# Kernel optimization log

Measured on AMD Instinct MI355X. Metric: run time of the kernel, lower is better.

The kernel has to match this reference:

```python
import jax, jax.numpy as jnp
import numpy as np

GN_GROUPS = 32
GN_EPS = 1e-5


def conv1x1(x, w, b):
    # x: [B,C,H,W], w: [O,C], b: [O]
    return jnp.einsum('bchw,oc->bohw', x, w) + b[None, :, None, None]


def maxpool2(x):
    B, C, H, W = x.shape
    return x.reshape(B, C, H // 2, 2, W // 2, 2).max(axis=(3, 5))


def group_norm(x, w, b, groups=GN_GROUPS, eps=GN_EPS):
    B, C, H, W = x.shape
    xg = x.reshape(B, groups, -1)
    m = xg.mean(axis=-1, keepdims=True)
    v = xg.var(axis=-1, keepdims=True)
    xn = ((xg - m) * jax.lax.rsqrt(v + eps)).reshape(B, C, H, W)
    return xn * w[None, :, None, None] + b[None, :, None, None]


def setup_inputs() -> dict:
    key = jax.random.key(0)
    ks = jax.random.split(key, 8)
    B, C, Ci, H, W = 4, 128, 64, 96, 96
    s_in = 1.0 / np.sqrt(C)
    s_ic = 1.0 / np.sqrt(Ci)
    return {
        'x': jax.random.normal(ks[0], (B, C, H, W), jnp.float32),
        'w_theta': jax.random.normal(ks[1], (Ci, C), jnp.float32) * s_in,
        'b_theta': jnp.zeros((Ci,), jnp.float32),
        'w_phi': jax.random.normal(ks[2], (Ci, C), jnp.float32) * s_in,
        'b_phi': jnp.zeros((Ci,), jnp.float32),
        'w_g': jax.random.normal(ks[3], (Ci, C), jnp.float32) * s_in,
        'b_g': jnp.zeros((Ci,), jnp.float32),
        'w_W': jax.random.normal(ks[4], (C, Ci), jnp.float32) * s_ic,
        'b_W': jnp.zeros((C,), jnp.float32),
        'gn_w': jnp.ones((C,), jnp.float32),
        'gn_b': jnp.zeros((C,), jnp.float32),
    }


def reference(x, w_theta, b_theta, w_phi, b_phi, w_g, b_g, w_W, b_W, gn_w, gn_b):
    B, C, H, W = x.shape
    Ci = w_theta.shape[0]
    # projections (1x1 convs); phi and g are 2x2 max-pooled (sub_sample=True)
    theta = conv1x1(x, w_theta, b_theta).reshape(B, Ci, H * W)          # [B,Ci,N]
    phi = maxpool2(conv1x1(x, w_phi, b_phi)).reshape(B, Ci, -1)         # [B,Ci,N']
    g = maxpool2(conv1x1(x, w_g, b_g)).reshape(B, Ci, -1)               # [B,Ci,N']
    # unscaled single-head attention
    f = jnp.einsum('bcn,bcm->bnm', theta, phi)                          # [B,N,N']
    f = jax.nn.softmax(f, axis=-1)
    y = jnp.einsum('bnm,bcm->bcn', f, g).reshape(B, Ci, H, W)           # [B,Ci,H,W]
    w_y = group_norm(conv1x1(y, w_W, b_W), gn_w, gn_b)
    return w_y + x
```

## Files before the change

kernel.cpp:

```cpp
#include <hip/hip_runtime.h>
#include <math.h>

#define B_ 4
#define C_ 128
#define CI_ 64
#define H_ 96
#define W_ 96
#define HW_ (H_*W_)
#define NP_ 2304
#define GROUPS_ 32
#define EPS_ 1e-5f
#define KVT_ 32
#define NT_ (NP_/KVT_)
#define NBLK_ 288

typedef _Float16 f16x8 __attribute__((ext_vector_type(8)));
typedef _Float16 f16x2 __attribute__((ext_vector_type(2)));
typedef __attribute__((ext_vector_type(4))) float f32x4;

__device__ inline f32x4 mfma16h(f16x8 a, f16x8 b, f32x4 c) {
    return __builtin_amdgcn_mfma_f32_16x16x32_f16(a, b, c, 0, 0, 0);
}
__device__ inline float h2f(unsigned short s) {
    return (float)__builtin_bit_cast(_Float16, s);
}
__device__ inline unsigned pk_f16(float a, float b) {
    return __builtin_bit_cast(unsigned, __builtin_amdgcn_cvt_pkrtz(a, b));
}
__device__ inline f16x8 pk8(float v0, float v1, float v2, float v3,
                            float v4, float v5, float v6, float v7) {
    uint4 u = { pk_f16(v0, v1), pk_f16(v2, v3), pk_f16(v4, v5), pk_f16(v6, v7) };
    return __builtin_bit_cast(f16x8, u);
}
__device__ inline unsigned short hmax4(unsigned short a, unsigned short b,
                                       unsigned short c, unsigned short d) {
    unsigned short m = (h2f(a) >= h2f(b)) ? a : b;
    unsigned short n = (h2f(c) >= h2f(d)) ? c : d;
    return (h2f(m) >= h2f(n)) ? m : n;
}
__device__ inline void gload_lds16(const void* g, void* l) {
    __builtin_amdgcn_global_load_lds(
        (const __attribute__((address_space(1))) void*)reinterpret_cast<uintptr_t>(g),
        (__attribute__((address_space(3))) void*)(unsigned)reinterpret_cast<uintptr_t>(l),
        16, 0, 0);
}

__global__ __launch_bounds__(256) void wprep_kernel(
    const float* __restrict__ w_theta, const float* __restrict__ w_phi,
    const float* __restrict__ w_g,     const float* __restrict__ w_W,
    unsigned short* __restrict__ Whall)
{
    const int idx = blockIdx.x * 256 + threadIdx.x;
    float v;
    if      (idx <  8192) v = w_theta[idx];
    else if (idx < 16384) v = w_phi[idx - 8192];
    else if (idx < 24576) v = w_g[idx - 16384];
    else                  v = w_W[idx - 24576];
    Whall[idx] = __builtin_bit_cast(unsigned short, (_Float16)v);
}

__global__ __launch_bounds__(128) void proj_kernel(
    const float* __restrict__ x, const unsigned short* __restrict__ Whall,
    const float* __restrict__ b_theta, const float* __restrict__ b_phi,
    const float* __restrict__ b_g,
    unsigned short* __restrict__ Qo, unsigned short* __restrict__ Ko,
    unsigned short* __restrict__ Vt)
{
    __shared__ __align__(16) unsigned short pb[2][16 * 72];

    const int t    = threadIdx.x;
    const int wv   = t >> 6;
    const int lane = t & 63;
    const int lr   = lane & 15;
    const int lg   = lane >> 4;
    const int b    = blockIdx.y;
    const int h0   = (blockIdx.x / 6) * 2;
    const int w0   = (blockIdx.x % 6) * 16;
    const int nb   = (h0 + wv) * W_ + w0;
    const int m0   = (h0 >> 1) * 48 + (w0 >> 1);

    const float* xb = x + (size_t)b * C_ * HW_ + nb + lr;
    f16x8 xa[4];
    #pragma unroll
    for (int u = 0; u < 4; ++u) {
        const float* p = xb + (size_t)(u * 32 + lg * 8) * HW_;
        xa[u] = pk8(p[0], p[(size_t)HW_], p[2 * (size_t)HW_], p[3 * (size_t)HW_],
                    p[4 * (size_t)HW_], p[5 * (size_t)HW_], p[6 * (size_t)HW_],
                    p[7 * (size_t)HW_]);
    }

    #pragma unroll
    for (int mat = 0; mat < 3; ++mat) {
        const unsigned short* Whp = Whall + mat * 8192;
        const float* bsel = (mat == 0) ? b_theta : (mat == 1) ? b_phi : b_g;

        f32x4 D[4];
        #pragma unroll
        for (int ct = 0; ct < 4; ++ct) D[ct] = (f32x4){0.f, 0.f, 0.f, 0.f};
        #pragma unroll
        for (int u = 0; u < 4; ++u)
            #pragma unroll
            for (int ct = 0; ct < 4; ++ct) {
                f16x8 wb = *(const f16x8*)&Whp[(ct * 16 + lr) * 128 + u * 32 + lg * 8];
                D[ct] = mfma16h(xa[u], wb, D[ct]);
            }

        #pragma unroll
        for (int ct = 0; ct < 4; ++ct) {
            const float bi = bsel[ct * 16 + lr];
            #pragma unroll
            for (int r2 = 0; r2 < 4; ++r2)
                pb[wv][(4 * lg + r2) * 72 + ct * 16 + lr] =
                    __builtin_bit_cast(unsigned short, (_Float16)(D[ct][r2] + bi));
        }

        if (mat == 0) {
            const int px = lane >> 2, ch = lane & 3;
            f16x8 y0 = *(const f16x8*)&pb[wv][px * 72 + ch * 16];
            f16x8 y1 = *(const f16x8*)&pb[wv][px * 72 + ch * 16 + 8];
            unsigned short* op = Qo + ((size_t)b * HW_ + nb + px) * CI_ + ch * 16;
            *(f16x8*)op       = y0;
            *(f16x8*)(op + 8) = y1;
        } else if (mat == 1) {
            __syncthreads();
            const int w = t >> 4, ci0 = (t & 15) * 4;
            unsigned short r[4];
            #pragma unroll
            for (int j = 0; j < 4; ++j) {
                const int ci = ci0 + j;
                r[j] = hmax4(pb[0][(2 * w) * 72 + ci], pb[0][(2 * w + 1) * 72 + ci],
                             pb[1][(2 * w) * 72 + ci], pb[1][(2 * w + 1) * 72 + ci]);
            }
            *(ushort4*)&Ko[((size_t)b * NP_ + m0 + w) * CI_ + ci0] =
                (ushort4){r[0], r[1], r[2], r[3]};
            __syncthreads();
        } else {
            __syncthreads();
            const int ci = t >> 1, pr = t & 1;
            #pragma unroll
            for (int j = 0; j < 4; ++j) {
                const int w = pr * 4 + j;
                unsigned short v = hmax4(
                    pb[0][(2 * w) * 72 + ci], pb[0][(2 * w + 1) * 72 + ci],
                    pb[1][(2 * w) * 72 + ci], pb[1][(2 * w + 1) * 72 + ci]);
                const int m  = m0 + w;
                const int ms = (m & ~31)
                             | (8 * ((m >> 2) & 3) + 4 * ((m >> 4) & 1) + (m & 3));
                Vt[((size_t)b * CI_ + ci) * NP_ + ms] = v;
            }
        }
    }
}

__global__ __launch_bounds__(128) void attn_kernel(
    const unsigned short* __restrict__ Qg, const unsigned short* __restrict__ Kg,
    const unsigned short* __restrict__ Vt, const unsigned short* __restrict__ wWh,
    const float* __restrict__ bW, unsigned short* __restrict__ Zh,
    float* __restrict__ gpart)
{
    __shared__ unsigned char Klds[2][4096];
    __shared__ unsigned char Vlds[2][4096];

    const int t    = threadIdx.x;
    const int wv   = t >> 6;
    const int lane = t & 63;
    const int lr   = lane & 15;
    const int lg   = lane >> 4;
    const int b    = blockIdx.y;
    const int q0   = blockIdx.x * 32 + wv * 16;

    const int krow = lane >> 3;
    const int kchk = (lane & 7) ^ krow;
    const int vrow = lane >> 2;
    const int vchk = (lane & 3) ^ (vrow & 3);

    const unsigned short* Kb = Kg + (size_t)b * NP_ * CI_;
    const unsigned short* Vb = Vt + (size_t)b * CI_ * NP_;

    f16x8 qf[2];
    #pragma unroll
    for (int u = 0; u < 2; ++u)
        qf[u] = *(const f16x8*)(Qg + ((size_t)b * HW_ + q0 + lr) * CI_ + u * 32 + lg * 8);

    f32x4 o_acc[4];
    #pragma unroll
    for (int dt = 0; dt < 4; ++dt) o_acc[dt] = (f32x4){0.f, 0.f, 0.f, 0.f};
    float mrun = -1e30f, lrun = 0.f;

#define STAGE(BUF, TT)                                                          \
    {                                                                           \
        const int kv0_ = (TT) * KVT_;                                           \
        if (wv == 0) {                                                          \
            _Pragma("unroll")                                                   \
            for (int i = 0; i < 4; ++i)                                         \
                gload_lds16(Kb + (size_t)(kv0_ + 8 * i + krow) * CI_ + kchk * 8,\
                            &Klds[BUF][i * 1024]);                              \
        } else {                                                                \
            _Pragma("unroll")                                                   \
            for (int i = 0; i < 4; ++i)                                         \
                gload_lds16(Vb + (size_t)(16 * i + vrow) * NP_ + kv0_ + vchk * 8,\
                            &Vlds[BUF][i * 1024]);                              \
        }                                                                       \
    }

#define COMPUTE(BUF)                                                            \
    {                                                                           \
        f16x8 kf[2][2];                                                         \
        _Pragma("unroll")                                                       \
        for (int u = 0; u < 2; ++u)                                             \
            _Pragma("unroll")                                                   \
            for (int k4 = 0; k4 < 2; ++k4)                                      \
                kf[u][k4] = *(const f16x8*)&Klds[BUF][(k4 * 16 + lr) * 128      \
                                + (((4 * u + lg) ^ (lr & 7)) << 4)];            \
        f32x4 s[2];                                                             \
        s[0] = (f32x4){0.f, 0.f, 0.f, 0.f};                                     \
        s[1] = (f32x4){0.f, 0.f, 0.f, 0.f};                                     \
        __builtin_amdgcn_s_setprio(1);                                          \
        _Pragma("unroll")                                                       \
        for (int u = 0; u < 2; ++u) {                                           \
            s[0] = mfma16h(kf[u][0], qf[u], s[0]);                              \
            s[1] = mfma16h(kf[u][1], qf[u], s[1]);                              \
        }                                                                       \
        __builtin_amdgcn_s_setprio(0);                                          \
        float tmax = fmaxf(fmaxf(fmaxf(s[0][0], s[0][1]),                       \
                                 fmaxf(s[0][2], s[0][3])),                      \
                           fmaxf(fmaxf(s[1][0], s[1][1]),                       \
                                 fmaxf(s[1][2], s[1][3])));                     \
        if (!__all(tmax <= mrun + 8.0f)) {                                      \
            tmax = fmaxf(tmax, __shfl_xor(tmax, 16));                           \
            tmax = fmaxf(tmax, __shfl_xor(tmax, 32));                           \
            const float mnew = fmaxf(mrun, tmax);                               \
            const float sc = __expf(mrun - mnew);                               \
            lrun *= sc;                                                         \
            _Pragma("unroll")                                                   \
            for (int r2 = 0; r2 < 4; ++r2) {                                    \
                const float scb = __shfl(sc, 4 * lg + r2);                      \
                _Pragma("unroll")                                               \
                for (int dt = 0; dt < 4; ++dt) o_acc[dt][r2] *= scb;            \
            }                                                                   \
            mrun = mnew;                                                        \
        }                                                                       \
        const float e00 = __expf(s[0][0] - mrun);                               \
        const float e01 = __expf(s[0][1] - mrun);                               \
        const float e02 = __expf(s[0][2] - mrun);                               \
        const float e03 = __expf(s[0][3] - mrun);                               \
        const float e10 = __expf(s[1][0] - mrun);                               \
        const float e11 = __expf(s[1][1] - mrun);                               \
        const float e12 = __expf(s[1][2] - mrun);                               \
        const float e13 = __expf(s[1][3] - mrun);                               \
        lrun += ((e00 + e01) + (e02 + e03)) + ((e10 + e11) + (e12 + e13));      \
        f16x8 pf = pk8(e00, e01, e02, e03, e10, e11, e12, e13);                 \
        __builtin_amdgcn_s_setprio(1);                                          \
        _Pragma("unroll")                                                       \
        for (int dt = 0; dt < 4; ++dt) {                                        \
            const int vrow_ = dt * 16 + lr;                                     \
            f16x8 vf = *(const f16x8*)&Vlds[BUF][vrow_ * 64                     \
                            + (((lg ^ (lr & 3))) << 4)];                        \
            o_acc[dt] = mfma16h(pf, vf, o_acc[dt]);                             \
        }                                                                       \
        __builtin_amdgcn_s_setprio(0);                                          \
    }

    STAGE(0, 0);
    STAGE(1, 1);

    for (int it = 0; it < NT_ / 2; ++it) {
        const int t0 = 2 * it;
        asm volatile("s_waitcnt vmcnt(4)" ::: "memory");
        __builtin_amdgcn_s_barrier();
        COMPUTE(0);
        __builtin_amdgcn_s_barrier();
        if (t0 + 2 < NT_) STAGE(0, t0 + 2);
        if (it == NT_ / 2 - 1) {
            asm volatile("s_waitcnt vmcnt(0)" ::: "memory");
        } else {
            asm volatile("s_waitcnt vmcnt(4)" ::: "memory");
        }
        __builtin_amdgcn_s_barrier();
        COMPUTE(1);
        __builtin_amdgcn_s_barrier();
        if (t0 + 3 < NT_) STAGE(1, t0 + 3);
    }

    float lt = lrun;
    lt += __shfl_xor(lt, 16);
    lt += __shfl_xor(lt, 32);
    unsigned short* yb = (unsigned short*)&Klds[wv][0];
    #pragma unroll
    for (int r2 = 0; r2 < 4; ++r2) {
        const float inv = 1.0f / __shfl(lt, 4 * lg + r2);
        #pragma unroll
        for (int dt = 0; dt < 4; ++dt)
            yb[(4 * lg + r2) * 72 + dt * 16 + lr] =
                __builtin_bit_cast(unsigned short, (_Float16)(o_acc[dt][r2] * inv));
    }

    float* wpart = (float*)&Vlds[0][0];
    f16x8 ya[2];
    #pragma unroll
    for (int u = 0; u < 2; ++u)
        ya[u] = *(const f16x8*)&yb[lr * 72 + u * 32 + lg * 8];

    unsigned short* Zb = Zh + (size_t)b * C_ * HW_ + q0 + lr;
    #pragma unroll
    for (int ot = 0; ot < 8; ++ot) {
        f32x4 D = (f32x4){0.f, 0.f, 0.f, 0.f};
        #pragma unroll
        for (int u = 0; u < 2; ++u) {
            f16x8 wa = *(const f16x8*)&wWh[(ot * 16 + lr) * CI_ + u * 32 + lg * 8];
            D = mfma16h(wa, ya[u], D);
        }
        float zs = 0.f, zq = 0.f;
        #pragma unroll
        for (int r2 = 0; r2 < 4; ++r2) {
            const int o = ot * 16 + 4 * lg + r2;
            const float z = D[r2] + bW[o];
            Zb[(size_t)o * HW_] = __builtin_bit_cast(unsigned short, (_Float16)z);
            zs += z;
            zq += z * z;
        }
        zs += __shfl_xor(zs, 1);  zq += __shfl_xor(zq, 1);
        zs += __shfl_xor(zs, 2);  zq += __shfl_xor(zq, 2);
        zs += __shfl_xor(zs, 4);  zq += __shfl_xor(zq, 4);
        zs += __shfl_xor(zs, 8);  zq += __shfl_xor(zq, 8);
        if (lr == 0) {
            wpart[(wv * 32 + ot * 4 + lg) * 2 + 0] = zs;
            wpart[(wv * 32 + ot * 4 + lg) * 2 + 1] = zq;
        }
    }
    __syncthreads();
    if (t < 64) {
        const int g = t >> 1, w = t & 1;
        const float v = wpart[(g) * 2 + w] + wpart[(32 + g) * 2 + w];
        gpart[(((size_t)b * NBLK_ + blockIdx.x) * 32 + g) * 2 + w] = v;
    }
#undef STAGE
#undef COMPUTE
}

__global__ __launch_bounds__(256) void final_kernel(
    const unsigned short* __restrict__ Zh, const float* __restrict__ xg,
    const float* __restrict__ gpart, const float* __restrict__ gnw,
    const float* __restrict__ gnb, float* __restrict__ out)
{
    __shared__ float red[256][2];
    const int t = threadIdx.x;
    const int c = blockIdx.x;
    const int b = blockIdx.y;
    const int zc = blockIdx.z;
    const int g = c >> 2;

    float v1 = 0.f, v2 = 0.f;
    for (int j = t; j < NBLK_; j += 256) {
        v1 += gpart[(((size_t)b * NBLK_ + j) * 32 + g) * 2 + 0];
        v2 += gpart[(((size_t)b * NBLK_ + j) * 32 + g) * 2 + 1];
    }
    red[t][0] = v1; red[t][1] = v2;
    __syncthreads();
    for (int off = 128; off > 0; off >>= 1) {
        if (t < off) { red[t][0] += red[t + off][0]; red[t][1] += red[t + off][1]; }
        __syncthreads();
    }
    const float invn = 1.0f / (4 * HW_);
    const float mean = red[0][0] * invn;
    const float var  = red[0][1] * invn - mean * mean;
    const float rstd = rsqrtf(var + EPS_);
    const float sc = rstd * gnw[c];
    const float sh = gnb[c] - mean * sc;

    const unsigned short* zp = Zh + ((size_t)b * C_ + c) * HW_;
    const float4* xp = (const float4*)(xg + ((size_t)b * C_ + c) * HW_);
    float4*       op = (float4*)(out + ((size_t)b * C_ + c) * HW_);
    #pragma unroll
    for (int i = 0; i < 3; ++i) {
        const int j = (zc * 3 + i) * 256 + t;
        const ushort4 zv = *(const ushort4*)(zp + (size_t)j * 4);
        const float4 xv = xp[j];
        float4 o;
        o.x = h2f(zv.x) * sc + sh + xv.x;
        o.y = h2f(zv.y) * sc + sh + xv.y;
        o.z = h2f(zv.z) * sc + sh + xv.z;
        o.w = h2f(zv.w) * sc + sh + xv.w;
        op[j] = o;
    }
}

extern "C" void kernel_launch(void* const* d_in, const int* in_sizes, int n_in,
                              void* d_out, int out_size, void* d_ws, size_t ws_size,
                              hipStream_t stream)
{
    const float* x       = (const float*)d_in[0];
    const float* w_theta = (const float*)d_in[1];
    const float* b_theta = (const float*)d_in[2];
    const float* w_phi   = (const float*)d_in[3];
    const float* b_phi   = (const float*)d_in[4];
    const float* w_g     = (const float*)d_in[5];
    const float* b_g     = (const float*)d_in[6];
    const float* w_W     = (const float*)d_in[7];
    const float* b_W     = (const float*)d_in[8];
    const float* gn_w    = (const float*)d_in[9];
    const float* gn_b    = (const float*)d_in[10];
    float* out = (float*)d_out;
    char* wsb  = (char*)d_ws;

    unsigned short* Q    = (unsigned short*)(wsb);
    unsigned short* K    = (unsigned short*)(wsb +  4718592);
    unsigned short* Vt   = (unsigned short*)(wsb +  5898240);
    float* gpart         = (float*)(wsb + 11796480);
    unsigned short* Zh   = (unsigned short*)(wsb + 16515072);
    unsigned short* Whall= (unsigned short*)(wsb + 35390464);
    unsigned short* wWh  = Whall + 24576;

    wprep_kernel<<<128, 256, 0, stream>>>(w_theta, w_phi, w_g, w_W, Whall);
    proj_kernel <<<dim3(288, B_), 128, 0, stream>>>(
        x, Whall, b_theta, b_phi, b_g, Q, K, Vt);
    attn_kernel <<<dim3(HW_ / 32, B_), 128, 0, stream>>>(
        Q, K, Vt, wWh, b_W, Zh, gpart);
    final_kernel<<<dim3(C_, B_, 3), 256, 0, stream>>>(Zh, x, gpart, gn_w, gn_b, out);
}
```

Before: 96.77 us.

## Fuse GroupNorm and residual into attention kernel via cooperative grid sync

The separate final kernel is removed. The attention kernel now keeps its W-projection outputs in registers, publishes per-block GroupNorm partial sums, and waits on a cooperative grid-wide barrier. After the barrier every block reduces the statistics, normalizes its own tile through LDS, adds the residual x and writes the output directly. This avoids the fp16 Z intermediate round trip through global memory and one kernel launch. In exchange it adds a grid barrier, requires all 1152 blocks to be co-resident, and raises register pressure.

```diff
diff --git a/kernel.cpp b/kernel.cpp
--- a/kernel.cpp
+++ b/kernel.cpp
@@ -1,5 +1,8 @@
 #include <hip/hip_runtime.h>
+#include <hip/hip_cooperative_groups.h>
 #include <math.h>
+
+namespace cg = cooperative_groups;
 
 #define B_ 4
 #define C_ 128
@@ -152,14 +155,19 @@
     }
 }
 
-__global__ __launch_bounds__(128) void attn_kernel(
+__global__ __launch_bounds__(128, 3) void attn_kernel(
     const unsigned short* __restrict__ Qg, const unsigned short* __restrict__ Kg,
     const unsigned short* __restrict__ Vt, const unsigned short* __restrict__ wWh,
-    const float* __restrict__ bW, unsigned short* __restrict__ Zh,
-    float* __restrict__ gpart)
+    const float* __restrict__ bW, const float* __restrict__ xg,
+    const float* __restrict__ gnw, const float* __restrict__ gnb,
+    float* __restrict__ gpart, float* __restrict__ out)
 {
-    __shared__ unsigned char Klds[2][4096];
-    __shared__ unsigned char Vlds[2][4096];
+    __shared__ __align__(16) unsigned char SMEM[16384];
+    __shared__ float sred[128];
+    __shared__ float mstat[32][2];
+    __shared__ float gwb[128][2];
+#define KLDS(BUF) (SMEM + (BUF) * 4096)
+#define VLDS(BUF) (SMEM + 8192 + (BUF) * 4096)
 
     const int t    = threadIdx.x;
     const int wv   = t >> 6;
@@ -169,6 +177,9 @@
     const int b    = blockIdx.y;
     const int q0   = blockIdx.x * 32 + wv * 16;
 
+    gwb[t][0] = gnw[t & 127];
+    gwb[t][1] = gnb[t & 127];
+
     const int krow = lane >> 3;
     const int kchk = (lane & 7) ^ krow;
     const int vrow = lane >> 2;
@@ -194,12 +205,12 @@
             _Pragma("unroll")                                                   \
             for (int i = 0; i < 4; ++i)                                         \
                 gload_lds16(Kb + (size_t)(kv0_ + 8 * i + krow) * CI_ + kchk * 8,\
-                            &Klds[BUF][i * 1024]);                              \
+                            KLDS(BUF) + i * 1024);                              \
         } else {                                                                \
             _Pragma("unroll")                                                   \
             for (int i = 0; i < 4; ++i)                                         \
                 gload_lds16(Vb + (size_t)(16 * i + vrow) * NP_ + kv0_ + vchk * 8,\
-                            &Vlds[BUF][i * 1024]);                              \
+                            VLDS(BUF) + i * 1024);                              \
         }                                                                       \
     }
 
@@ -210,8 +221,8 @@
         for (int u = 0; u < 2; ++u)                                             \
             _Pragma("unroll")                                                   \
             for (int k4 = 0; k4 < 2; ++k4)                                      \
-                kf[u][k4] = *(const f16x8*)&Klds[BUF][(k4 * 16 + lr) * 128      \
-                                + (((4 * u + lg) ^ (lr & 7)) << 4)];            \
+                kf[u][k4] = *(const f16x8*)(KLDS(BUF) + (k4 * 16 + lr) * 128    \
+                                + (((4 * u + lg) ^ (lr & 7)) << 4));            \
         f32x4 s[2];                                                             \
         s[0] = (f32x4){0.f, 0.f, 0.f, 0.f};                                     \
         s[1] = (f32x4){0.f, 0.f, 0.f, 0.f};                                     \
@@ -254,8 +265,8 @@
         _Pragma("unroll")                                                       \
         for (int dt = 0; dt < 4; ++dt) {                                        \
             const int vrow_ = dt * 16 + lr;                                     \
-            f16x8 vf = *(const f16x8*)&Vlds[BUF][vrow_ * 64                     \
-                            + (((lg ^ (lr & 3))) << 4)];                        \
+            f16x8 vf = *(const f16x8*)(VLDS(BUF) + vrow_ * 64                   \
+                            + (((lg ^ (lr & 3))) << 4));                        \
             o_acc[dt] = mfma16h(pf, vf, o_acc[dt]);                             \
         }                                                                       \
         __builtin_amdgcn_s_setprio(0);                                          \
@@ -285,7 +296,7 @@
     float lt = lrun;
     lt += __shfl_xor(lt, 16);
     lt += __shfl_xor(lt, 32);
-    unsigned short* yb = (unsigned short*)&Klds[wv][0];
+    unsigned short* yb = (unsigned short*)(SMEM + wv * 4096);
     #pragma unroll
     for (int r2 = 0; r2 < 4; ++r2) {
         const float inv = 1.0f / __shfl(lt, 4 * lg + r2);
@@ -295,13 +306,13 @@
                 __builtin_bit_cast(unsigned short, (_Float16)(o_acc[dt][r2] * inv));
     }
 
-    float* wpart = (float*)&Vlds[0][0];
+    float* wpart = (float*)(SMEM + 8192);
     f16x8 ya[2];
     #pragma unroll
     for (int u = 0; u < 2; ++u)
         ya[u] = *(const f16x8*)&yb[lr * 72 + u * 32 + lg * 8];
 
-    unsigned short* Zb = Zh + (size_t)b * C_ * HW_ + q0 + lr;
+    float zreg[8][4];
     #pragma unroll
     for (int ot = 0; ot < 8; ++ot) {
         f32x4 D = (f32x4){0.f, 0.f, 0.f, 0.f};
@@ -315,7 +326,7 @@
         for (int r2 = 0; r2 < 4; ++r2) {
             const int o = ot * 16 + 4 * lg + r2;
             const float z = D[r2] + bW[o];
-            Zb[(size_t)o * HW_] = __builtin_bit_cast(unsigned short, (_Float16)z);
+            zreg[ot][r2] = z;
             zs += z;
             zq += z * z;
         }
@@ -331,58 +342,62 @@
     __syncthreads();
     if (t < 64) {
         const int g = t >> 1, w = t & 1;
-        const float v = wpart[(g) * 2 + w] + wpart[(32 + g) * 2 + w];
+        const float v = wpart[g * 2 + w] + wpart[(32 + g) * 2 + w];
         gpart[(((size_t)b * NBLK_ + blockIdx.x) * 32 + g) * 2 + w] = v;
+    }
+
+    __threadfence();
+    cg::this_grid().sync();
+
+    {
+        const int gw = t & 63;
+        const float* gp = gpart + (size_t)b * NBLK_ * 64 + gw;
+        float acc = 0.f;
+        for (int j = (t >> 6); j < NBLK_; j += 2)
+            acc += gp[(size_t)j * 64];
+        sred[t] = acc;
+    }
+    __syncthreads();
+    if (t < 64) ((float*)mstat)[t] = sred[t] + sred[t + 64];
+    __syncthreads();
+    if (t < 32) {
+        const float invn = 1.0f / (4 * HW_);
+        const float m = mstat[t][0] * invn;
+        const float v = mstat[t][1] * invn - m * m;
+        mstat[t][0] = m;
+        mstat[t][1] = rsqrtf(v + EPS_);
+    }
+    __syncthreads();
+
+    float* zb = (float*)SMEM;
+    #pragma unroll
+    for (int ot = 0; ot < 8; ++ot)
+        #pragma unroll
+        for (int r2 = 0; r2 < 4; ++r2) {
+            const int o = ot * 16 + 4 * lg + r2;
+            const int g = o >> 2;
+            const float sc = mstat[g][1] * gwb[o][0];
+            const float sh = gwb[o][1] - mstat[g][0] * sc;
+            zb[o * 32 + wv * 16 + lr] = zreg[ot][r2] * sc + sh;
+        }
+    __syncthreads();
+
+    {
+        const size_t rb = (size_t)b * C_ * HW_ + blockIdx.x * 32;
+        const float* xr = xg + rb;
+        float* orow = out + rb;
+        #pragma unroll
+        for (int i = 0; i < 32; ++i) {
+            const int flat = i * 128 + t;
+            const int o  = flat >> 5;
+            const int px = flat & 31;
+            orow[(size_t)o * HW_ + px] = zb[flat] + xr[(size_t)o * HW_ + px];
+        }
     }
 #undef STAGE
 #undef COMPUTE
-}
-
-__global__ __launch_bounds__(256) void final_kernel(
-    const unsigned short* __restrict__ Zh, const float* __restrict__ xg,
-    const float* __restrict__ gpart, const float* __restrict__ gnw,
-    const float* __restrict__ gnb, float* __restrict__ out)
-{
-    __shared__ float red[256][2];
-    const int t = threadIdx.x;
-    const int c = blockIdx.x;
-    const int b = blockIdx.y;
-    const int zc = blockIdx.z;
-    const int g = c >> 2;
-
-    float v1 = 0.f, v2 = 0.f;
-    for (int j = t; j < NBLK_; j += 256) {
-        v1 += gpart[(((size_t)b * NBLK_ + j) * 32 + g) * 2 + 0];
-        v2 += gpart[(((size_t)b * NBLK_ + j) * 32 + g) * 2 + 1];
-    }
-    red[t][0] = v1; red[t][1] = v2;
-    __syncthreads();
-    for (int off = 128; off > 0; off >>= 1) {
-        if (t < off) { red[t][0] += red[t + off][0]; red[t][1] += red[t + off][1]; }
-        __syncthreads();
-    }
-    const float invn = 1.0f / (4 * HW_);
-    const float mean = red[0][0] * invn;
-    const float var  = red[0][1] * invn - mean * mean;
-    const float rstd = rsqrtf(var + EPS_);
-    const float sc = rstd * gnw[c];
-    const float sh = gnb[c] - mean * sc;
-
-    const unsigned short* zp = Zh + ((size_t)b * C_ + c) * HW_;
-    const float4* xp = (const float4*)(xg + ((size_t)b * C_ + c) * HW_);
-    float4*       op = (float4*)(out + ((size_t)b * C_ + c) * HW_);
-    #pragma unroll
-    for (int i = 0; i < 3; ++i) {
-        const int j = (zc * 3 + i) * 256 + t;
-        const ushort4 zv = *(const ushort4*)(zp + (size_t)j * 4);
-        const float4 xv = xp[j];
-        float4 o;
-        o.x = h2f(zv.x) * sc + sh + xv.x;
-        o.y = h2f(zv.y) * sc + sh + xv.y;
-        o.z = h2f(zv.z) * sc + sh + xv.z;
-        o.w = h2f(zv.w) * sc + sh + xv.w;
-        op[j] = o;
-    }
+#undef KLDS
+#undef VLDS
 }
 
 extern "C" void kernel_launch(void* const* d_in, const int* in_sizes, int n_in,
@@ -407,14 +422,16 @@
     unsigned short* K    = (unsigned short*)(wsb +  4718592);
     unsigned short* Vt   = (unsigned short*)(wsb +  5898240);
     float* gpart         = (float*)(wsb + 11796480);
-    unsigned short* Zh   = (unsigned short*)(wsb + 16515072);
     unsigned short* Whall= (unsigned short*)(wsb + 35390464);
-    unsigned short* wWh  = Whall + 24576;
+    const unsigned short* wWh = Whall + 24576;
 
     wprep_kernel<<<128, 256, 0, stream>>>(w_theta, w_phi, w_g, w_W, Whall);
     proj_kernel <<<dim3(288, B_), 128, 0, stream>>>(
         x, Whall, b_theta, b_phi, b_g, Q, K, Vt);
-    attn_kernel <<<dim3(HW_ / 32, B_), 128, 0, stream>>>(
-        Q, K, Vt, wWh, b_W, Zh, gpart);
-    final_kernel<<<dim3(C_, B_, 3), 256, 0, stream>>>(Zh, x, gpart, gn_w, gn_b, out);
-}
+
+    void* args[] = { (void*)&Q, (void*)&K, (void*)&Vt, (void*)&wWh,
+                     (void*)&b_W, (void*)&x, (void*)&gn_w, (void*)&gn_b,
+                     (void*)&gpart, (void*)&out };
+    hipLaunchCooperativeKernel((void*)attn_kernel, dim3(HW_ / 32, B_),
+                               dim3(128), args, 0, stream);
+}
```

New measurement: 336.5 us. 248% more time.
